# Kernel tuning notes

Hardware: AMD Instinct MI355X
Metric: run time of the kernel (lower is better)

The kernel has to match this reference:

```python
import jax, jax.numpy as jnp
import numpy as np

B, S, A, H, E = 8192, 256, 64, 1024, 8
IN = S + A
OUT = S + 1


def setup_inputs() -> dict:
    key = jax.random.key(0)
    ks = jax.random.split(key, 8)
    state = jax.random.normal(ks[0], (B, S), dtype=jnp.float32)
    action = jax.random.normal(ks[1], (B, A), dtype=jnp.float32)
    idx = jax.random.randint(ks[2], (B,), 0, E, dtype=jnp.int32)
    # Kaiming-ish scaling to keep activations sane
    W1 = jax.random.normal(ks[3], (E, IN, H), dtype=jnp.float32) / np.sqrt(IN)
    b1 = jnp.zeros((E, H), dtype=jnp.float32)
    W2 = jax.random.normal(ks[4], (E, H, H), dtype=jnp.float32) / np.sqrt(H)
    b2 = jnp.zeros((E, H), dtype=jnp.float32)
    W3 = jax.random.normal(ks[5], (E, H, OUT), dtype=jnp.float32) / np.sqrt(H)
    b3 = jnp.zeros((E, OUT), dtype=jnp.float32)
    return {"state": state, "action": action, "idx": idx,
            "W1": W1, "b1": b1, "W2": W2, "b2": b2, "W3": W3, "b3": b3}


def reference(state, action, idx, W1, b1, W2, b2, W3, b3):
    # Dense-MoE style: run all E experts on the full batch, then select the
    # per-sample expert output chosen by idx (matches masked gather/scatter
    # in the torch predict loop).
    x = jnp.concatenate([state, action], axis=-1)                  # [B, IN]
    h = jax.nn.relu(jnp.einsum('bi,eih->beh', x, W1) + b1)         # [B, E, H]
    h = jax.nn.relu(jnp.einsum('beh,ehk->bek', h, W2) + b2)        # [B, E, H]
    out = jnp.einsum('beh,eho->beo', h, W3) + b3                   # [B, E, S+1]
    sel = jnp.take_along_axis(out, idx[:, None, None], axis=1)[:, 0]  # [B, S+1]
    s_dim = state.shape[-1]
    delta = sel[:, :s_dim]
    reward = sel[:, s_dim:]
    next_state = state + delta
    return next_state, reward
```

## Files before the change

### kernel.cpp

```cpp
#include <hip/hip_runtime.h>
#include <stdint.h>

#define B_SZ   8192
#define IN_DIM 320
#define H_DIM  1024
#define E_NUM  8
#define OUT_DIM 257
#define MAXT1  (B_SZ / 128 + E_NUM)
#define MAXT2  (B_SZ / 64 + E_NUM)

typedef __bf16 bf16x8 __attribute__((ext_vector_type(8)));
typedef float  f32x4  __attribute__((ext_vector_type(4)));
typedef float  f32x4v __attribute__((ext_vector_type(4)));

typedef unsigned int __attribute__((address_space(1))) as1_uint;
typedef unsigned int __attribute__((address_space(3))) as3_uint;

__device__ __forceinline__ void gload_lds16(const void* g, void* l) {
    __builtin_amdgcn_global_load_lds((const as1_uint*)g, (as3_uint*)l, 16, 0, 0);
}

__device__ __forceinline__ unsigned short f2bf(float f) {
    unsigned int u = __float_as_uint(f);
    return (unsigned short)((u + 0x7fffu + ((u >> 16) & 1u)) >> 16);
}

__global__ __launch_bounds__(256)
void k_prep(const float* __restrict__ state, const float* __restrict__ action,
            const int* __restrict__ idx,
            const float* __restrict__ W1, const float* __restrict__ W2,
            const float* __restrict__ W3,
            unsigned short* __restrict__ xb, unsigned short* __restrict__ w1t,
            unsigned short* __restrict__ w2t, unsigned short* __restrict__ w3t,
            int* __restrict__ order,
            int* __restrict__ te,  int* __restrict__ tp0, int* __restrict__ tcnt,
            int* __restrict__ te2, int* __restrict__ tp2, int* __restrict__ tc2) {
    __shared__ int scnt[16][E_NUM];
    int bid = blockIdx.x, tid = threadIdx.x;

    if (bid == 0) {
        int shard = tid & 15;
        if (tid < 128) ((int*)scnt)[tid] = 0;
        __syncthreads();
        for (int b = tid; b < B_SZ; b += 256) atomicAdd(&scnt[shard][idx[b]], 1);
        __syncthreads();
        if (tid == 0) {
            int pos = 0, t1 = 0, t2 = 0;
            for (int e = 0; e < E_NUM; e++) {
                int start = pos;
                for (int s = 0; s < 16; s++) { int c = scnt[s][e]; scnt[s][e] = pos; pos += c; }
                int tot = pos - start;
                for (int st = 0; st < tot; st += 128) {
                    te[t1] = e; tp0[t1] = start + st; tcnt[t1] = min(128, tot - st); t1++;
                }
                for (int st = 0; st < tot; st += 64) {
                    te2[t2] = e; tp2[t2] = start + st; tc2[t2] = min(64, tot - st); t2++;
                }
            }
            for (; t1 < MAXT1; t1++) { te[t1] = 0; tp0[t1] = 0; tcnt[t1] = 0; }
            for (; t2 < MAXT2; t2++) { te2[t2] = 0; tp2[t2] = 0; tc2[t2] = 0; }
        }
        __syncthreads();
        for (int b = tid; b < B_SZ; b += 256) {
            int e = idx[b];
            int p = atomicAdd(&scnt[shard][e], 1);
            order[p] = b;
        }
        return;
    }

    if (bid <= 2560) {
        int q = (bid - 1) * 256 + tid;
        int b = q / 80, j = q % 80;
        float4 v = (j < 64) ? ((const float4*)state)[b * 64 + j]
                            : ((const float4*)action)[b * 16 + (j - 64)];
        ushort4 o;
        o.x = f2bf(v.x); o.y = f2bf(v.y); o.z = f2bf(v.z); o.w = f2bf(v.w);
        ((ushort4*)xb)[q] = o;
        return;
    }

    if (bid < 5761) {
        int e, kt, nt, K, Nsrc, dstRows; bool vec;
        const float* src; unsigned short* dst;
        if (bid < 3201) {
            int r = bid - 2561; e = r / 80; int m = r % 80; kt = m / 16; nt = m % 16;
            K = IN_DIM; Nsrc = H_DIM; dstRows = H_DIM; src = W1; dst = w1t; vec = true;
        } else if (bid < 5249) {
            int r = bid - 3201; e = r / 256; int m = r % 256; kt = m / 16; nt = m % 16;
            K = H_DIM; Nsrc = H_DIM; dstRows = H_DIM; src = W2; dst = w2t; vec = true;
        } else {
            int r = bid - 5249; e = r / 64; int m = r % 64; kt = m / 4; nt = m % 4;
            K = H_DIM; Nsrc = OUT_DIM; dstRows = 320; src = W3; dst = w3t; vec = false;
        }
        int k0 = kt * 64, n0 = nt * 64;
        const float* s = src + (size_t)e * K * Nsrc;
        unsigned short* d = dst + (size_t)e * dstRows * K;
        int kc4 = (tid & 15) * 4;
        int nc4 = (tid >> 4) * 4;
        const float* sp = s + (size_t)(k0 + kc4) * Nsrc + n0 + nc4;
        f32x4v v[4];
        if (vec) {
#pragma unroll
            for (int i = 0; i < 4; i++)
                v[i] = *(const f32x4v*)(sp + (size_t)i * Nsrc);
        } else {
#pragma unroll
            for (int i = 0; i < 4; i++)
#pragma unroll
                for (int j = 0; j < 4; j++)
                    v[i][j] = sp[(size_t)i * Nsrc + j];
        }
#pragma unroll
        for (int j = 0; j < 4; j++) {
            ushort4 o;
            o.x = f2bf(v[0][j]); o.y = f2bf(v[1][j]);
            o.z = f2bf(v[2][j]); o.w = f2bf(v[3][j]);
            *(ushort4*)&d[(size_t)(n0 + nc4 + j) * K + k0 + kc4] = o;
        }
        return;
    }

    int i = (bid - 5761) * 256 + tid;
    int e = i >> 10, k = i & 1023;
    w3t[((size_t)e * 320 + 256) * H_DIM + k] =
        f2bf(W3[((size_t)e * H_DIM + k) * OUT_DIM + 256]);
}

template <int K, int TM, int TN, bool GATHER, int MODE>
__global__ __launch_bounds__(256, 2)
void k_gemm(const unsigned short* __restrict__ Abase,
            const unsigned short* __restrict__ Wt, int wtRows,
            const float* __restrict__ bias, int bstride,
            unsigned short* __restrict__ Hout,
            float* __restrict__ Out, const float* __restrict__ state,
            const int* __restrict__ order,
            const int* __restrict__ te, const int* __restrict__ tp0,
            const int* __restrict__ tcnt) {
    constexpr int NI  = K / 32;
    constexpr int WM  = TM / 2, MF = WM / 16;
    constexpr int WN  = TN / 2, NF = WN / 16;
    constexpr int ABY = TM * 64;
    constexpr int BBY = TN * 64;
    constexpr int STG = ABY + BBY;
    __shared__ __align__(16) char lds[2 * STG];

    int t = blockIdx.x;
    int cnt = tcnt[t];
    if (cnt == 0) return;
    int e = te[t], p0 = tp0[t];
    int n0 = blockIdx.y * TN;
    int tid = threadIdx.x;
    int w = tid >> 6, lane = tid & 63;
    int wm = w >> 1, wn = w & 1;

    int r0 = tid >> 2;
    int cg = (tid & 3) ^ ((r0 >> 1) & 3);
    int rc0 = r0 < cnt ? r0 : cnt - 1;
    long a0 = GATHER ? order[p0 + rc0] : (p0 + rc0);
    const unsigned short* aP0 = Abase + (size_t)a0 * K + cg * 8;
    const unsigned short* aP1 = aP0;
    if (TM == 128) {
        int rc1 = (r0 + 64) < cnt ? (r0 + 64) : cnt - 1;
        long a1 = GATHER ? order[p0 + rc1] : (p0 + rc1);
        aP1 = Abase + (size_t)a1 * K + cg * 8;
    }
    const unsigned short* bP0 = Wt + ((size_t)e * wtRows + n0 + r0) * K + cg * 8;
    const unsigned short* bP1 = bP0 + (size_t)64 * K;

    auto stage = [&](int k0s, int sb) {
        gload_lds16(aP0 + k0s, lds + sb + tid * 16);
        if (TM == 128)
            gload_lds16(aP1 + k0s, lds + sb + 4096 + tid * 16);
        gload_lds16(bP0 + k0s, lds + sb + ABY + tid * 16);
        if (TN == 128)
            gload_lds16(bP1 + k0s, lds + sb + ABY + 4096 + tid * 16);
    };

    f32x4 acc[MF][NF];
#pragma unroll
    for (int i = 0; i < MF; i++)
#pragma unroll
        for (int j = 0; j < NF; j++) acc[i][j] = (f32x4)0.f;

    const int fm   = lane & 15;
    const int kc   = lane >> 4;
    const int koff = ((kc ^ ((fm >> 1) & 3)) * 8);

    stage(0, 0);
    for (int it = 0; it < NI; ++it) {
        __syncthreads();
        if (it + 1 < NI) stage((it + 1) * 32, ((it + 1) & 1) * STG);
        const unsigned short* Ls = (const unsigned short*)(lds + (it & 1) * STG);
        const unsigned short* As = Ls + wm * WM * 32;
        const unsigned short* Bs = Ls + ABY / 2 + wn * WN * 32;

        bf16x8 af[MF], bf[NF];
#pragma unroll
        for (int i = 0; i < MF; i++)
            af[i] = *(const bf16x8*)&As[(i * 16 + fm) * 32 + koff];
#pragma unroll
        for (int j = 0; j < NF; j++)
            bf[j] = *(const bf16x8*)&Bs[(j * 16 + fm) * 32 + koff];
#pragma unroll
        for (int i = 0; i < MF; i++)
#pragma unroll
            for (int j = 0; j < NF; j++)
                acc[i][j] = __builtin_amdgcn_mfma_f32_16x16x32_bf16(
                    af[i], bf[j], acc[i][j], 0, 0, 0);
    }

    int col = lane & 15, rq = lane >> 4;
#pragma unroll
    for (int j = 0; j < NF; j++) {
        int n = n0 + wn * WN + j * 16 + col;
        float bv = (MODE == 0) ? bias[e * bstride + n]
                               : ((n <= 256) ? bias[e * bstride + n] : 0.f);
#pragma unroll
        for (int i = 0; i < MF; i++) {
#pragma unroll
            for (int rr = 0; rr < 4; rr++) {
                int m = wm * WM + i * 16 + rq * 4 + rr;
                if (m < cnt) {
                    float v = acc[i][j][rr] + bv;
                    if (MODE == 0) {
                        Hout[(size_t)(p0 + m) * H_DIM + n] = f2bf(fmaxf(v, 0.f));
                    } else {
                        int row = order[p0 + m];
                        if (n < 256) {
                            size_t o = (size_t)row * 256 + n;
                            Out[o] = state[o] + v;
                        } else if (n == 256) {
                            Out[(size_t)B_SZ * 256 + row] = v;
                        }
                    }
                }
            }
        }
    }
}

extern "C" void kernel_launch(void* const* d_in, const int* in_sizes, int n_in,
                              void* d_out, int out_size, void* d_ws, size_t ws_size,
                              hipStream_t stream) {
    const float* state  = (const float*)d_in[0];
    const float* action = (const float*)d_in[1];
    const int*   idx    = (const int*)d_in[2];
    const float* W1     = (const float*)d_in[3];
    const float* b1     = (const float*)d_in[4];
    const float* W2     = (const float*)d_in[5];
    const float* b2     = (const float*)d_in[6];
    const float* W3     = (const float*)d_in[7];
    const float* b3     = (const float*)d_in[8];
    float* out = (float*)d_out;

    char* ws = (char*)d_ws;
    size_t off = 0;
    auto alloc = [&](size_t bytes) -> void* {
        void* p = ws + off;
        off = (off + bytes + 255) & ~(size_t)255;
        return p;
    };
    unsigned short* xb  = (unsigned short*)alloc((size_t)B_SZ * IN_DIM * 2);
    unsigned short* w1t = (unsigned short*)alloc((size_t)E_NUM * H_DIM * IN_DIM * 2);
    unsigned short* w2t = (unsigned short*)alloc((size_t)E_NUM * H_DIM * H_DIM * 2);
    unsigned short* w3t = (unsigned short*)alloc((size_t)E_NUM * 320 * H_DIM * 2);
    unsigned short* h1  = (unsigned short*)alloc((size_t)B_SZ * H_DIM * 2);
    unsigned short* h2  = (unsigned short*)alloc((size_t)B_SZ * H_DIM * 2);
    int* order = (int*)alloc(B_SZ * 4);
    int* te    = (int*)alloc(MAXT1 * 4);
    int* tp0   = (int*)alloc(MAXT1 * 4);
    int* tcnt  = (int*)alloc(MAXT1 * 4);
    int* te2   = (int*)alloc(MAXT2 * 4);
    int* tp2   = (int*)alloc(MAXT2 * 4);
    int* tc2   = (int*)alloc(MAXT2 * 4);

    k_prep<<<5793, 256, 0, stream>>>(state, action, idx, W1, W2, W3,
                                     xb, w1t, w2t, w3t, order,
                                     te, tp0, tcnt, te2, tp2, tc2);

    k_gemm<IN_DIM, 128, 64, true, 0><<<dim3(MAXT1, 16), 256, 0, stream>>>(
        xb, w1t, H_DIM, b1, H_DIM, h1, nullptr, nullptr, order, te, tp0, tcnt);
    k_gemm<H_DIM, 128, 128, false, 0><<<dim3(MAXT1, 8), 256, 0, stream>>>(
        h1, w2t, H_DIM, b2, H_DIM, h2, nullptr, nullptr, order, te, tp0, tcnt);
    k_gemm<H_DIM, 64, 64, false, 1><<<dim3(MAXT2, 5), 256, 0, stream>>>(
        h2, w3t, 320, b3, OUT_DIM, nullptr, out, state, order, te2, tp2, tc2);
}
```

Measured before the change: 229.8 us.

## Fuse prep and three expert GEMMs into one persistent cooperative kernel

Replaces the four kernel launches with a single persistent cooperative kernel. It does the prep work (bucketing, bf16 conversion, weight transposes) and then the three grouped GEMM stages, separated by grid-wide syncs. The weight transpose now goes through a padded LDS tile so both global reads and writes are coalesced, and the first GEMM uses 128x128 tiles instead of 128x64. This removes launch gaps and tail effects between stages, at the cost of grid.sync overhead and a persistent grid of at most 512 blocks, which may underfill some stages. A fallback to separate launches remains if the cooperative launch fails.

Measured after the change: 477.4 us. 108% more time.

```diff
diff --git a/kernel.cpp b/kernel.cpp
--- a/kernel.cpp
+++ b/kernel.cpp
@@ -1,17 +1,19 @@
 #include <hip/hip_runtime.h>
+#include <hip/hip_cooperative_groups.h>
 #include <stdint.h>
+
+namespace cg = cooperative_groups;
 
 #define B_SZ   8192
 #define IN_DIM 320
 #define H_DIM  1024
 #define E_NUM  8
 #define OUT_DIM 257
-#define MAXT1  (B_SZ / 128 + E_NUM)
-#define MAXT2  (B_SZ / 64 + E_NUM)
+#define MAXT1  72
+#define MAXT2  136
 
 typedef __bf16 bf16x8 __attribute__((ext_vector_type(8)));
 typedef float  f32x4  __attribute__((ext_vector_type(4)));
-typedef float  f32x4v __attribute__((ext_vector_type(4)));
 
 typedef unsigned int __attribute__((address_space(1))) as1_uint;
 typedef unsigned int __attribute__((address_space(3))) as3_uint;
@@ -25,147 +27,44 @@
     return (unsigned short)((u + 0x7fffu + ((u >> 16) & 1u)) >> 16);
 }
 
-__global__ __launch_bounds__(256)
-void k_prep(const float* __restrict__ state, const float* __restrict__ action,
-            const int* __restrict__ idx,
-            const float* __restrict__ W1, const float* __restrict__ W2,
-            const float* __restrict__ W3,
-            unsigned short* __restrict__ xb, unsigned short* __restrict__ w1t,
-            unsigned short* __restrict__ w2t, unsigned short* __restrict__ w3t,
-            int* __restrict__ order,
-            int* __restrict__ te,  int* __restrict__ tp0, int* __restrict__ tcnt,
-            int* __restrict__ te2, int* __restrict__ tp2, int* __restrict__ tc2) {
-    __shared__ int scnt[16][E_NUM];
-    int bid = blockIdx.x, tid = threadIdx.x;
-
-    if (bid == 0) {
-        int shard = tid & 15;
-        if (tid < 128) ((int*)scnt)[tid] = 0;
-        __syncthreads();
-        for (int b = tid; b < B_SZ; b += 256) atomicAdd(&scnt[shard][idx[b]], 1);
-        __syncthreads();
-        if (tid == 0) {
-            int pos = 0, t1 = 0, t2 = 0;
-            for (int e = 0; e < E_NUM; e++) {
-                int start = pos;
-                for (int s = 0; s < 16; s++) { int c = scnt[s][e]; scnt[s][e] = pos; pos += c; }
-                int tot = pos - start;
-                for (int st = 0; st < tot; st += 128) {
-                    te[t1] = e; tp0[t1] = start + st; tcnt[t1] = min(128, tot - st); t1++;
-                }
-                for (int st = 0; st < tot; st += 64) {
-                    te2[t2] = e; tp2[t2] = start + st; tc2[t2] = min(64, tot - st); t2++;
-                }
-            }
-            for (; t1 < MAXT1; t1++) { te[t1] = 0; tp0[t1] = 0; tcnt[t1] = 0; }
-            for (; t2 < MAXT2; t2++) { te2[t2] = 0; tp2[t2] = 0; tc2[t2] = 0; }
-        }
-        __syncthreads();
-        for (int b = tid; b < B_SZ; b += 256) {
-            int e = idx[b];
-            int p = atomicAdd(&scnt[shard][e], 1);
-            order[p] = b;
-        }
-        return;
-    }
-
-    if (bid <= 2560) {
-        int q = (bid - 1) * 256 + tid;
-        int b = q / 80, j = q % 80;
-        float4 v = (j < 64) ? ((const float4*)state)[b * 64 + j]
-                            : ((const float4*)action)[b * 16 + (j - 64)];
-        ushort4 o;
-        o.x = f2bf(v.x); o.y = f2bf(v.y); o.z = f2bf(v.z); o.w = f2bf(v.w);
-        ((ushort4*)xb)[q] = o;
-        return;
-    }
-
-    if (bid < 5761) {
-        int e, kt, nt, K, Nsrc, dstRows; bool vec;
-        const float* src; unsigned short* dst;
-        if (bid < 3201) {
-            int r = bid - 2561; e = r / 80; int m = r % 80; kt = m / 16; nt = m % 16;
-            K = IN_DIM; Nsrc = H_DIM; dstRows = H_DIM; src = W1; dst = w1t; vec = true;
-        } else if (bid < 5249) {
-            int r = bid - 3201; e = r / 256; int m = r % 256; kt = m / 16; nt = m % 16;
-            K = H_DIM; Nsrc = H_DIM; dstRows = H_DIM; src = W2; dst = w2t; vec = true;
-        } else {
-            int r = bid - 5249; e = r / 64; int m = r % 64; kt = m / 4; nt = m % 4;
-            K = H_DIM; Nsrc = OUT_DIM; dstRows = 320; src = W3; dst = w3t; vec = false;
-        }
-        int k0 = kt * 64, n0 = nt * 64;
-        const float* s = src + (size_t)e * K * Nsrc;
-        unsigned short* d = dst + (size_t)e * dstRows * K;
-        int kc4 = (tid & 15) * 4;
-        int nc4 = (tid >> 4) * 4;
-        const float* sp = s + (size_t)(k0 + kc4) * Nsrc + n0 + nc4;
-        f32x4v v[4];
-        if (vec) {
-#pragma unroll
-            for (int i = 0; i < 4; i++)
-                v[i] = *(const f32x4v*)(sp + (size_t)i * Nsrc);
-        } else {
-#pragma unroll
-            for (int i = 0; i < 4; i++)
-#pragma unroll
-                for (int j = 0; j < 4; j++)
-                    v[i][j] = sp[(size_t)i * Nsrc + j];
-        }
-#pragma unroll
-        for (int j = 0; j < 4; j++) {
-            ushort4 o;
-            o.x = f2bf(v[0][j]); o.y = f2bf(v[1][j]);
-            o.z = f2bf(v[2][j]); o.w = f2bf(v[3][j]);
-            *(ushort4*)&d[(size_t)(n0 + nc4 + j) * K + k0 + kc4] = o;
-        }
-        return;
-    }
-
-    int i = (bid - 5761) * 256 + tid;
-    int e = i >> 10, k = i & 1023;
-    w3t[((size_t)e * 320 + 256) * H_DIM + k] =
-        f2bf(W3[((size_t)e * H_DIM + k) * OUT_DIM + 256]);
-}
-
 template <int K, int TM, int TN, bool GATHER, int MODE>
-__global__ __launch_bounds__(256, 2)
-void k_gemm(const unsigned short* __restrict__ Abase,
-            const unsigned short* __restrict__ Wt, int wtRows,
-            const float* __restrict__ bias, int bstride,
-            unsigned short* __restrict__ Hout,
-            float* __restrict__ Out, const float* __restrict__ state,
-            const int* __restrict__ order,
-            const int* __restrict__ te, const int* __restrict__ tp0,
-            const int* __restrict__ tcnt) {
+__device__ __forceinline__ void gemm_tile(
+    char* lds, int t, int ny,
+    const unsigned short* __restrict__ Abase,
+    const unsigned short* __restrict__ Wt, int wtRows,
+    const float* __restrict__ bias, int bstride,
+    unsigned short* __restrict__ Hout,
+    float* __restrict__ Out, const float* __restrict__ state,
+    const int* __restrict__ order,
+    const int* __restrict__ te, const int* __restrict__ tp0,
+    const int* __restrict__ tcnt) {
     constexpr int NI  = K / 32;
     constexpr int WM  = TM / 2, MF = WM / 16;
     constexpr int WN  = TN / 2, NF = WN / 16;
     constexpr int ABY = TM * 64;
     constexpr int BBY = TN * 64;
     constexpr int STG = ABY + BBY;
-    __shared__ __align__(16) char lds[2 * STG];
-
-    int t = blockIdx.x;
+
     int cnt = tcnt[t];
     if (cnt == 0) return;
     int e = te[t], p0 = tp0[t];
-    int n0 = blockIdx.y * TN;
+    int n0 = ny * TN;
     int tid = threadIdx.x;
     int w = tid >> 6, lane = tid & 63;
     int wm = w >> 1, wn = w & 1;
 
     int r0 = tid >> 2;
-    int cg = (tid & 3) ^ ((r0 >> 1) & 3);
+    int cg2 = (tid & 3) ^ ((r0 >> 1) & 3);
     int rc0 = r0 < cnt ? r0 : cnt - 1;
     long a0 = GATHER ? order[p0 + rc0] : (p0 + rc0);
-    const unsigned short* aP0 = Abase + (size_t)a0 * K + cg * 8;
+    const unsigned short* aP0 = Abase + (size_t)a0 * K + cg2 * 8;
     const unsigned short* aP1 = aP0;
     if (TM == 128) {
         int rc1 = (r0 + 64) < cnt ? (r0 + 64) : cnt - 1;
         long a1 = GATHER ? order[p0 + rc1] : (p0 + rc1);
-        aP1 = Abase + (size_t)a1 * K + cg * 8;
-    }
-    const unsigned short* bP0 = Wt + ((size_t)e * wtRows + n0 + r0) * K + cg * 8;
+        aP1 = Abase + (size_t)a1 * K + cg2 * 8;
+    }
+    const unsigned short* bP0 = Wt + ((size_t)e * wtRows + ny * TN + r0) * K + cg2 * 8;
     const unsigned short* bP1 = bP0 + (size_t)64 * K;
 
     auto stage = [&](int k0s, int sb) {
@@ -213,7 +112,7 @@
     int col = lane & 15, rq = lane >> 4;
 #pragma unroll
     for (int j = 0; j < NF; j++) {
-        int n = n0 + wn * WN + j * 16 + col;
+        int n = ny * TN + wn * WN + j * 16 + col;
         float bv = (MODE == 0) ? bias[e * bstride + n]
                                : ((n <= 256) ? bias[e * bstride + n] : 0.f);
 #pragma unroll
@@ -240,6 +139,193 @@
     }
 }
 
+__device__ __forceinline__ void prep_bucket(
+    char* smem, const int* __restrict__ idx, int* __restrict__ order,
+    int* __restrict__ te1, int* __restrict__ tp1, int* __restrict__ tc1,
+    int* __restrict__ te2, int* __restrict__ tp2, int* __restrict__ tc2) {
+    int (*scnt)[E_NUM] = (int(*)[E_NUM])smem;
+    int tid = threadIdx.x;
+    int shard = tid & 15;
+    if (tid < 128) ((int*)scnt)[tid] = 0;
+    __syncthreads();
+    for (int b = tid; b < B_SZ; b += 256) atomicAdd(&scnt[shard][idx[b]], 1);
+    __syncthreads();
+    if (tid == 0) {
+        int pos = 0, t1 = 0, t2 = 0;
+        for (int e = 0; e < E_NUM; e++) {
+            int start = pos;
+            for (int s = 0; s < 16; s++) { int c = scnt[s][e]; scnt[s][e] = pos; pos += c; }
+            int tot = pos - start;
+            for (int st = 0; st < tot; st += 128) {
+                te1[t1] = e; tp1[t1] = start + st; tc1[t1] = min(128, tot - st); t1++;
+            }
+            for (int st = 0; st < tot; st += 64) {
+                te2[t2] = e; tp2[t2] = start + st; tc2[t2] = min(64, tot - st); t2++;
+            }
+        }
+        for (; t1 < MAXT1; t1++) { te1[t1] = 0; tp1[t1] = 0; tc1[t1] = 0; }
+        for (; t2 < MAXT2; t2++) { te2[t2] = 0; tp2[t2] = 0; tc2[t2] = 0; }
+    }
+    __syncthreads();
+    for (int b = tid; b < B_SZ; b += 256) {
+        int e = idx[b];
+        int p = atomicAdd(&scnt[shard][e], 1);
+        order[p] = b;
+    }
+}
+
+__device__ __forceinline__ void prep_item(
+    char* smem, int item,
+    const float* __restrict__ state, const float* __restrict__ action,
+    const float* __restrict__ W1, const float* __restrict__ W2,
+    const float* __restrict__ W3,
+    unsigned short* __restrict__ xb, unsigned short* __restrict__ w1t,
+    unsigned short* __restrict__ w2t, unsigned short* __restrict__ w3t) {
+    int tid = threadIdx.x;
+    if (item < 2560) {
+        int q = item * 256 + tid;
+        int b = q / 80, j = q % 80;
+        float4 v = (j < 64) ? ((const float4*)state)[b * 64 + j]
+                            : ((const float4*)action)[b * 16 + (j - 64)];
+        ushort4 o;
+        o.x = f2bf(v.x); o.y = f2bf(v.y); o.z = f2bf(v.z); o.w = f2bf(v.w);
+        ((ushort4*)xb)[q] = o;
+    } else if (item < 5760) {
+        unsigned short (*tileU)[65] = (unsigned short(*)[65])smem;
+        int it2 = item - 2560;
+        int e, kt, nt, K, Nsrc, dstRows; bool vec;
+        const float* src; unsigned short* dst;
+        if (it2 < 640) {
+            e = it2 / 80; int m = it2 % 80; kt = m / 16; nt = m % 16;
+            K = IN_DIM; Nsrc = H_DIM; dstRows = H_DIM; src = W1; dst = w1t; vec = true;
+        } else if (it2 < 2688) {
+            int r = it2 - 640; e = r / 256; int m = r % 256; kt = m / 16; nt = m % 16;
+            K = H_DIM; Nsrc = H_DIM; dstRows = H_DIM; src = W2; dst = w2t; vec = true;
+        } else {
+            int r = it2 - 2688; e = r / 64; int m = r % 64; kt = m / 4; nt = m % 4;
+            K = H_DIM; Nsrc = OUT_DIM; dstRows = 320; src = W3; dst = w3t; vec = false;
+        }
+        int k0 = kt * 64, n0 = nt * 64;
+        const float* s = src + (size_t)e * K * Nsrc;
+        unsigned short* d = dst + (size_t)e * dstRows * K;
+        int c4 = (tid & 15) * 4;
+        int rb = tid >> 4;
+#pragma unroll
+        for (int p = 0; p < 4; p++) {
+            int r = rb + p * 16;
+            const float* sp = s + (size_t)(k0 + r) * Nsrc + n0 + c4;
+            float4 v;
+            if (vec) v = *(const float4*)sp;
+            else { v.x = sp[0]; v.y = sp[1]; v.z = sp[2]; v.w = sp[3]; }
+            tileU[r][c4 + 0] = f2bf(v.x);
+            tileU[r][c4 + 1] = f2bf(v.y);
+            tileU[r][c4 + 2] = f2bf(v.z);
+            tileU[r][c4 + 3] = f2bf(v.w);
+        }
+        __syncthreads();
+#pragma unroll
+        for (int p = 0; p < 4; p++) {
+            int n = rb + p * 16;
+            ushort4 o;
+            o.x = tileU[c4 + 0][n];
+            o.y = tileU[c4 + 1][n];
+            o.z = tileU[c4 + 2][n];
+            o.w = tileU[c4 + 3][n];
+            *(ushort4*)&d[(size_t)(n0 + n) * K + k0 + c4] = o;
+        }
+        __syncthreads();
+    } else {
+        int i = (item - 5760) * 256 + tid;
+        int e = i >> 10, k = i & 1023;
+        w3t[((size_t)e * 320 + 256) * H_DIM + k] =
+            f2bf(W3[((size_t)e * H_DIM + k) * OUT_DIM + 256]);
+    }
+}
+
+__global__ __launch_bounds__(256, 2)
+void k_fused(const float* __restrict__ state, const float* __restrict__ action,
+             const int* __restrict__ idx,
+             const float* __restrict__ W1, const float* __restrict__ b1,
+             const float* __restrict__ W2, const float* __restrict__ b2,
+             const float* __restrict__ W3, const float* __restrict__ b3,
+             float* __restrict__ out,
+             unsigned short* __restrict__ xb, unsigned short* __restrict__ w1t,
+             unsigned short* __restrict__ w2t, unsigned short* __restrict__ w3t,
+             unsigned short* __restrict__ h1, unsigned short* __restrict__ h2,
+             int* __restrict__ order,
+             int* __restrict__ te1, int* __restrict__ tp1, int* __restrict__ tc1,
+             int* __restrict__ te2, int* __restrict__ tp2, int* __restrict__ tc2) {
+    __shared__ __align__(16) char smem[32768];
+    cg::grid_group grid = cg::this_grid();
+    int bid = blockIdx.x;
+    int nb  = gridDim.x;
+
+    if (bid == 0) {
+        prep_bucket(smem, idx, order, te1, tp1, tc1, te2, tp2, tc2);
+    } else {
+        for (int item = bid - 1; item < 5792; item += nb - 1)
+            prep_item(smem, item, state, action, W1, W2, W3, xb, w1t, w2t, w3t);
+    }
+
+    __threadfence();
+    grid.sync();
+
+    for (int tl = bid; tl < MAXT1 * 8; tl += nb)
+        gemm_tile<IN_DIM, 128, 128, true, 0>(smem, tl % MAXT1, tl / MAXT1,
+            xb, w1t, H_DIM, b1, H_DIM, h1, nullptr, nullptr,
+            order, te1, tp1, tc1);
+
+    __threadfence();
+    grid.sync();
+
+    for (int tl = bid; tl < MAXT1 * 8; tl += nb)
+        gemm_tile<H_DIM, 128, 128, false, 0>(smem, tl % MAXT1, tl / MAXT1,
+            h1, w2t, H_DIM, b2, H_DIM, h2, nullptr, nullptr,
+            order, te1, tp1, tc1);
+
+    __threadfence();
+    grid.sync();
+
+    for (int tl = bid; tl < MAXT2 * 5; tl += nb)
+        gemm_tile<H_DIM, 64, 64, false, 1>(smem, tl % MAXT2, tl / MAXT2,
+            h2, w3t, 320, b3, OUT_DIM, nullptr, out, state,
+            order, te2, tp2, tc2);
+}
+
+__global__ __launch_bounds__(256)
+void k_prep_fb(const float* __restrict__ state, const float* __restrict__ action,
+               const int* __restrict__ idx,
+               const float* __restrict__ W1, const float* __restrict__ W2,
+               const float* __restrict__ W3,
+               unsigned short* __restrict__ xb, unsigned short* __restrict__ w1t,
+               unsigned short* __restrict__ w2t, unsigned short* __restrict__ w3t,
+               int* __restrict__ order,
+               int* __restrict__ te1, int* __restrict__ tp1, int* __restrict__ tc1,
+               int* __restrict__ te2, int* __restrict__ tp2, int* __restrict__ tc2) {
+    __shared__ __align__(16) char smem[8448];
+    int bid = blockIdx.x;
+    if (bid == 0)
+        prep_bucket(smem, idx, order, te1, tp1, tc1, te2, tp2, tc2);
+    else
+        prep_item(smem, bid - 1, state, action, W1, W2, W3, xb, w1t, w2t, w3t);
+}
+
+template <int K, int TM, int TN, bool GATHER, int MODE>
+__global__ __launch_bounds__(256, 2)
+void k_gemm_fb(const unsigned short* __restrict__ Abase,
+               const unsigned short* __restrict__ Wt, int wtRows,
+               const float* __restrict__ bias, int bstride,
+               unsigned short* __restrict__ Hout,
+               float* __restrict__ Out, const float* __restrict__ state,
+               const int* __restrict__ order,
+               const int* __restrict__ te, const int* __restrict__ tp0,
+               const int* __restrict__ tcnt) {
+    __shared__ __align__(16) char lds[2 * (TM * 64 + TN * 64)];
+    gemm_tile<K, TM, TN, GATHER, MODE>(lds, blockIdx.x, blockIdx.y,
+        Abase, Wt, wtRows, bias, bstride, Hout, Out, state,
+        order, te, tp0, tcnt);
+}
+
 extern "C" void kernel_launch(void* const* d_in, const int* in_sizes, int n_in,
                               void* d_out, int out_size, void* d_ws, size_t ws_size,
                               hipStream_t stream) {
@@ -268,21 +354,43 @@
     unsigned short* h1  = (unsigned short*)alloc((size_t)B_SZ * H_DIM * 2);
     unsigned short* h2  = (unsigned short*)alloc((size_t)B_SZ * H_DIM * 2);
     int* order = (int*)alloc(B_SZ * 4);
-    int* te    = (int*)alloc(MAXT1 * 4);
-    int* tp0   = (int*)alloc(MAXT1 * 4);
-    int* tcnt  = (int*)alloc(MAXT1 * 4);
+    int* te1   = (int*)alloc(MAXT1 * 4);
+    int* tp1   = (int*)alloc(MAXT1 * 4);
+    int* tc1   = (int*)alloc(MAXT1 * 4);
     int* te2   = (int*)alloc(MAXT2 * 4);
     int* tp2   = (int*)alloc(MAXT2 * 4);
     int* tc2   = (int*)alloc(MAXT2 * 4);
 
-    k_prep<<<5793, 256, 0, stream>>>(state, action, idx, W1, W2, W3,
-                                     xb, w1t, w2t, w3t, order,
-                                     te, tp0, tcnt, te2, tp2, tc2);
-
-    k_gemm<IN_DIM, 128, 64, true, 0><<<dim3(MAXT1, 16), 256, 0, stream>>>(
-        xb, w1t, H_DIM, b1, H_DIM, h1, nullptr, nullptr, order, te, tp0, tcnt);
-    k_gemm<H_DIM, 128, 128, false, 0><<<dim3(MAXT1, 8), 256, 0, stream>>>(
-        h1, w2t, H_DIM, b2, H_DIM, h2, nullptr, nullptr, order, te, tp0, tcnt);
-    k_gemm<H_DIM, 64, 64, false, 1><<<dim3(MAXT2, 5), 256, 0, stream>>>(
-        h2, w3t, 320, b3, OUT_DIM, nullptr, out, state, order, te2, tp2, tc2);
-}
+    int perCU = 0;
+    hipError_t qerr = hipOccupancyMaxActiveBlocksPerMultiprocessor(
+        &perCU, (const void*)k_fused, 256, 0);
+    int grid = 512;
+    if (qerr == hipSuccess && perCU >= 1) {
+        int cap = perCU * 256;
+        if (cap < grid) grid = cap;
+    }
+
+    void* args[] = {
+        (void*)&state, (void*)&action, (void*)&idx,
+        (void*)&W1, (void*)&b1, (void*)&W2, (void*)&b2, (void*)&W3, (void*)&b3,
+        (void*)&out,
+        (void*)&xb, (void*)&w1t, (void*)&w2t, (void*)&w3t,
+        (void*)&h1, (void*)&h2,
+        (void*)&order, (void*)&te1, (void*)&tp1, (void*)&tc1,
+        (void*)&te2, (void*)&tp2, (void*)&tc2
+    };
+    hipError_t lerr = hipLaunchCooperativeKernel((const void*)k_fused,
+                                                 dim3(grid), dim3(256),
+                                                 args, 0, stream);
+    if (lerr != hipSuccess) {
+        k_prep_fb<<<5793, 256, 0, stream>>>(state, action, idx, W1, W2, W3,
+                                            xb, w1t, w2t, w3t, order,
+                                            te1, tp1, tc1, te2, tp2, tc2);
+        k_gemm_fb<IN_DIM, 128, 128, true, 0><<<dim3(MAXT1, 8), 256, 0, stream>>>(
+            xb, w1t, H_DIM, b1, H_DIM, h1, nullptr, nullptr, order, te1, tp1, tc1);
+        k_gemm_fb<H_DIM, 128, 128, false, 0><<<dim3(MAXT1, 8), 256, 0, stream>>>(
+            h1, w2t, H_DIM, b2, H_DIM, h2, nullptr, nullptr, order, te1, tp1, tc1);
+        k_gemm_fb<H_DIM, 64, 64, false, 1><<<dim3(MAXT2, 5), 256, 0, stream>>>(
+            h2, w3t, 320, b3, OUT_DIM, nullptr, out, state, order, te2, tp2, tc2);
+    }
+}
```
